# Performance work log

Measured on AMD Instinct MI355X. Metric: run time of the kernel, lower is better.

Reference implementation:

```python
import jax, jax.numpy as jnp
import numpy as np

N_NODES = 50000
N_EDGES = 800000
T_SEQ = 2048
H = 128  # LSTM hidden size


def _lstm_dir(x, w_ih, w_hh, b, reverse):
    # x: [T, Din]; torch gate order: i, f, g, o
    xg = x @ w_ih.T + b  # [T, 4H] precomputed input contribution
    h0 = jnp.zeros((H,), x.dtype)

    def step(carry, g_t):
        h, c = carry
        g = g_t + h @ w_hh.T
        i, f, gg, o = jnp.split(g, 4)
        i = jax.nn.sigmoid(i); f = jax.nn.sigmoid(f)
        gg = jnp.tanh(gg); o = jax.nn.sigmoid(o)
        c = f * c + i * gg
        h = o * jnp.tanh(c)
        return (h, c), h

    _, hs = jax.lax.scan(step, (h0, h0), xg, reverse=reverse)
    return hs  # [T, H], time-aligned with x


def _bilstm(x, layer_params):
    for (wif, whf, bf, wir, whr, br) in layer_params:
        hf = _lstm_dir(x, wif, whf, bf, reverse=False)
        hr = _lstm_dir(x, wir, whr, br, reverse=True)
        x = jnp.concatenate([hf, hr], axis=-1)
    return x  # [T, 2H]


def _forward(g_mol, feat_seq, edge_src, edge_dst, edge_weight, smiles_kmer,
             w_ih_l0, w_hh_l0, b_ih_l0, b_hh_l0,
             w_ih_l0_r, w_hh_l0_r, b_ih_l0_r, b_hh_l0_r,
             w_ih_l1, w_hh_l1, b_ih_l1, b_hh_l1,
             w_ih_l1_r, w_hh_l1_r, b_ih_l1_r, b_hh_l1_r,
             W1, b1, W2, b2,
             fc1_w, fc1_b, fc2_w, fc2_b, fc3_w, fc3_b, fc4_w, fc4_b):
    n = feat_seq.shape[0]
    # ---- BiLSTM encoder over the (unbatched) molecule sequence [T,17] ----
    layer_params = [
        (w_ih_l0, w_hh_l0, b_ih_l0 + b_hh_l0, w_ih_l0_r, w_hh_l0_r, b_ih_l0_r + b_hh_l0_r),
        (w_ih_l1, w_hh_l1, b_ih_l1 + b_hh_l1, w_ih_l1_r, w_hh_l1_r, b_ih_l1_r + b_hh_l1_r),
    ]
    lstm_out = _bilstm(g_mol, layer_params)              # [T, 256]
    g_mol_vec = lstm_out.mean(axis=0, keepdims=True)     # [1, 256] (mean over dim 0, keepdim)

    # ---- GraphConv 1 (norm='none'): weighted sum-aggregate src->dst, then linear ----
    msg = edge_weight[:, None] * feat_seq[edge_src]                # [E, 128]
    agg = jax.ops.segment_sum(msg, edge_dst, num_segments=n)      # [N, 128]
    h = jax.nn.relu(agg @ W1 + b1)
    # ---- GraphConv 2 ----
    msg2 = edge_weight[:, None] * h[edge_src]                      # [E, 128]
    agg2 = jax.ops.segment_sum(msg2, edge_dst, num_segments=n)    # [N, 128]
    h2 = agg2 @ W2 + b2                                            # [N, 256]
    hg_seq = h2.mean(axis=0, keepdims=True)                        # [1, 256] single-graph mean_nodes

    # ---- concat + MLP head ----
    features = jnp.concatenate([hg_seq, g_mol_vec, smiles_kmer], axis=1)  # [1, 1150]
    out = jax.nn.relu(features @ fc1_w.T + fc1_b)
    out = jax.nn.relu(out @ fc2_w.T + fc2_b)
    out = jax.nn.relu(out @ fc3_w.T + fc3_b)
    out = out @ fc4_w.T + fc4_b
    return out  # [1, 1]


def setup_inputs():
    key = jax.random.key(0)
    ks = iter(jax.random.split(key, 48))

    def rn(shape, s=0.05):
        return jax.random.normal(next(ks), shape, dtype=jnp.float32) * s

    inp = {}
    inp["g_mol"] = jax.random.normal(next(ks), (T_SEQ, 17), dtype=jnp.float32)
    inp["feat_seq"] = jax.random.normal(next(ks), (N_NODES, 128), dtype=jnp.float32)
    inp["edge_src"] = jax.random.randint(next(ks), (N_EDGES,), 0, N_NODES)
    inp["edge_dst"] = jax.random.randint(next(ks), (N_EDGES,), 0, N_NODES)
    inp["edge_weight"] = jax.random.uniform(next(ks), (N_EDGES,), dtype=jnp.float32)
    inp["smiles_kmer"] = jax.random.normal(next(ks), (1, 638), dtype=jnp.float32)
    for l, din in ((0, 17), (1, 2 * H)):
        for suf in ("", "_r"):
            inp[f"w_ih_l{l}{suf}"] = rn((4 * H, din))
            inp[f"w_hh_l{l}{suf}"] = rn((4 * H, H))
            inp[f"b_ih_l{l}{suf}"] = rn((4 * H,))
            inp[f"b_hh_l{l}{suf}"] = rn((4 * H,))
    inp["W1"] = rn((128, 128)); inp["b1"] = jnp.zeros((128,), jnp.float32)
    inp["W2"] = rn((128, 256)); inp["b2"] = jnp.zeros((256,), jnp.float32)
    inp["fc1_w"] = rn((575, 1150)); inp["fc1_b"] = jnp.zeros((575,), jnp.float32)
    inp["fc2_w"] = rn((256, 575)); inp["fc2_b"] = jnp.zeros((256,), jnp.float32)
    inp["fc3_w"] = rn((64, 256)); inp["fc3_b"] = jnp.zeros((64,), jnp.float32)
    inp["fc4_w"] = rn((1, 64)); inp["fc4_b"] = jnp.zeros((1,), jnp.float32)
    return inp


def reference(g_mol, feat_seq, edge_src, edge_dst, edge_weight, smiles_kmer,
              w_ih_l0, w_hh_l0, b_ih_l0, b_hh_l0,
              w_ih_l0_r, w_hh_l0_r, b_ih_l0_r, b_hh_l0_r,
              w_ih_l1, w_hh_l1, b_ih_l1, b_hh_l1,
              w_ih_l1_r, w_hh_l1_r, b_ih_l1_r, b_hh_l1_r,
              W1, b1, W2, b2,
              fc1_w, fc1_b, fc2_w, fc2_b, fc3_w, fc3_b, fc4_w, fc4_b):
    return _forward(g_mol, feat_seq, edge_src, edge_dst, edge_weight, smiles_kmer,
                    w_ih_l0, w_hh_l0, b_ih_l0, b_hh_l0,
                    w_ih_l0_r, w_hh_l0_r, b_ih_l0_r, b_hh_l0_r,
                    w_ih_l1, w_hh_l1, b_ih_l1, b_hh_l1,
                    w_ih_l1_r, w_hh_l1_r, b_ih_l1_r, b_hh_l1_r,
                    W1, b1, W2, b2,
                    fc1_w, fc1_b, fc2_w, fc2_b, fc3_w, fc3_b, fc4_w, fc4_b)
```

## Files before the change

kernel.cpp:

```cpp
#include <hip/hip_runtime.h>
#include <hip/hip_bf16.h>

#define T_SEQ 2048
#define HID 128
#define G4 512
#define N_NODES 50000
#define N_EDGES 800000

typedef float f32x4 __attribute__((ext_vector_type(4)));
typedef _Float16 f16x2 __attribute__((ext_vector_type(2)));
typedef _Float16 f16x8 __attribute__((ext_vector_type(8)));

__device__ __forceinline__ float fast_sigmoid(float x) {
    return 1.0f / (1.0f + __expf(-x));
}
__device__ __forceinline__ float fast_tanh(float x) {
    return 1.0f - 2.0f / (__expf(2.0f * x) + 1.0f);
}

__device__ __forceinline__ float dot2_f16(float bits_w, f16x2 h2, float acc) {
    f16x2 w2 = __builtin_bit_cast(f16x2, bits_w);
#if __has_builtin(__builtin_amdgcn_fdot2)
    return __builtin_amdgcn_fdot2(w2, h2, acc, false);
#else
    asm("v_dot2_f32_f16 %0, %1, %2, %0" : "+v"(acc) : "v"(w2), "v"(h2));
    return acc;
#endif
}

__global__ void xg0_kernel(const float* __restrict__ g_mol,
                           const float* __restrict__ wf, const float* __restrict__ bfi, const float* __restrict__ bfh,
                           const float* __restrict__ wr, const float* __restrict__ bri, const float* __restrict__ brh,
                           float* __restrict__ xg_f, float* __restrict__ xg_r)
{
    int gid = blockIdx.x * blockDim.x + threadIdx.x;
    int j = gid & (G4 - 1);
    int rest = gid >> 9;
    int t = rest & (T_SEQ - 1);
    int dir = rest >> 11;
    const float* w  = dir ? wr  : wf;
    const float* bi = dir ? bri : bfi;
    const float* bh = dir ? brh : bfh;
    float* xg = dir ? xg_r : xg_f;
    const float* x  = g_mol + t * 17;
    const float* wj = w + j * 17;
    float acc = bi[j] + bh[j];
    #pragma unroll
    for (int k = 0; k < 17; ++k) acc += x[k] * wj[k];
    xg[t * G4 + j] = acc;
}

struct ScanSmem {
    _Float16 h16[2][HID] __attribute__((aligned(16)));
    float g[G4];
    float part[G4];
};

#define B8(M) M(0,0,1,2,3) M(1,4,5,6,7) M(2,8,9,10,11) M(3,12,13,14,15) \
              M(4,16,17,18,19) M(5,20,21,22,23) M(6,24,25,26,27) M(7,28,29,30,31)
#define P32(M) M(0) M(1) M(2) M(3) M(4) M(5) M(6) M(7) M(8) M(9) M(10) M(11) \
               M(12) M(13) M(14) M(15) M(16) M(17) M(18) M(19) M(20) M(21) M(22) \
               M(23) M(24) M(25) M(26) M(27) M(28) M(29) M(30) M(31)

__device__ __forceinline__ void lstm_scan_dev(ScanSmem* sm, int dir,
                                              const float* __restrict__ xg,
                                              const float* __restrict__ whh,
                                              float* __restrict__ out,
                                              float* __restrict__ gvec, int write_out)
{
    const int tid = threadIdx.x;
    const int j = tid & (G4 - 1);
    const int half = tid >> 9;

    const float* wptr = whh + j * HID + half * 64;

#define DECL_PK(p) float apk##p; { \
    f16x2 pk_ = { (_Float16)wptr[2*(p)], (_Float16)wptr[2*(p)+1] }; \
    float bits_ = __builtin_bit_cast(float, pk_); \
    asm volatile("v_accvgpr_write_b32 %0, %1" : "=a"(apk##p) : "v"(bits_)); }
    P32(DECL_PK)
#undef DECL_PK

    if (tid < HID) sm->h16[0][tid] = (_Float16)0.0f;
    float c = 0.0f;
    float msum = 0.0f;
    __syncthreads();

    int t0 = dir ? (T_SEQ - 1) : 0;
    float xv = (half == 0) ? xg[t0 * G4 + j] : 0.0f;

    int pp = 0;
    for (int s = 0; s < T_SEQ; ++s) {
        int s2 = (s + 1 < T_SEQ) ? (s + 1) : s;
        int t      = dir ? (T_SEQ - 1 - s)  : s;
        int t_next = dir ? (T_SEQ - 1 - s2) : s2;
        float xv_n = (half == 0) ? xg[t_next * G4 + j] : 0.0f;

        const f16x8* h16v = reinterpret_cast<const f16x8*>(&sm->h16[pp][half * 64]);
        float acc0 = 0.f, acc1 = 0.f, acc2 = 0.f, acc3 = 0.f;
#define DOT_BLK(i, q0, q1, q2, q3) { f16x8 hv = h16v[i]; float b0_, b1_, b2_, b3_; \
        asm volatile("v_accvgpr_read_b32 %0, %1" : "=v"(b0_) : "a"(apk##q0)); \
        asm volatile("v_accvgpr_read_b32 %0, %1" : "=v"(b1_) : "a"(apk##q1)); \
        asm volatile("v_accvgpr_read_b32 %0, %1" : "=v"(b2_) : "a"(apk##q2)); \
        asm volatile("v_accvgpr_read_b32 %0, %1" : "=v"(b3_) : "a"(apk##q3)); \
        f16x2 h0_ = { hv[0], hv[1] }, h1_ = { hv[2], hv[3] }; \
        f16x2 h2_ = { hv[4], hv[5] }, h3_ = { hv[6], hv[7] }; \
        acc0 = dot2_f16(b0_, h0_, acc0); acc1 = dot2_f16(b1_, h1_, acc1); \
        acc2 = dot2_f16(b2_, h2_, acc2); acc3 = dot2_f16(b3_, h3_, acc3); }
        B8(DOT_BLK)
#undef DOT_BLK
        float p = (acc0 + acc1) + (acc2 + acc3);
        if (half) sm->part[j] = p;
        else      sm->g[j] = p + xv;
        __syncthreads();
        if (tid < HID) {
            float ig = fast_sigmoid(sm->g[tid]           + sm->part[tid]);
            float fg = fast_sigmoid(sm->g[HID + tid]     + sm->part[HID + tid]);
            float gg = fast_tanh(   sm->g[2 * HID + tid] + sm->part[2 * HID + tid]);
            float og = fast_sigmoid(sm->g[3 * HID + tid] + sm->part[3 * HID + tid]);
            c = fg * c + ig * gg;
            float hh = og * fast_tanh(c);
            sm->h16[pp ^ 1][tid] = (_Float16)hh;
            if (write_out) out[t * HID + tid] = hh;
            msum += hh;
        }
        __syncthreads();
        pp ^= 1;
        xv = xv_n;
    }
    if (gvec != nullptr && tid < HID) gvec[dir * HID + tid] = msum * (1.0f / (float)T_SEQ);
}

#define SCAT_BLOCKS ((N_EDGES * 32) / 1024)
__global__ __launch_bounds__(1024, 1)
void combined1(const float* __restrict__ xg_f, const float* __restrict__ xg_r,
               const float* __restrict__ whh_f, const float* __restrict__ whh_r,
               float* __restrict__ out_f, float* __restrict__ out_r,
               const int* __restrict__ esrc, const int* __restrict__ edst,
               const float* __restrict__ ew, const float* __restrict__ feat,
               float* __restrict__ agg)
{
    __shared__ ScanSmem ssm;
    __shared__ float pad_iso[19456];
    volatile float* vpad = pad_iso;
    vpad[threadIdx.x] = 0.0f;
    int bid = blockIdx.x;
    if (bid < 2) {
        lstm_scan_dev(&ssm, bid, bid ? xg_r : xg_f, bid ? whh_r : whh_f,
                      bid ? out_r : out_f, nullptr, 1);
        return;
    }
    int gid = (bid - 2) * 1024 + threadIdx.x;
    int e = gid >> 5;
    int c = gid & 31;
    int s = esrc[e], d = edst[e];
    float w = ew[e];
    float4 v = reinterpret_cast<const float4*>(feat)[(long)s * 32 + c];
    float* ap = agg + (long)d * HID + (c << 2);
    atomicAdd(ap + 0, w * v.x);
    atomicAdd(ap + 1, w * v.y);
    atomicAdd(ap + 2, w * v.z);
    atomicAdd(ap + 3, w * v.w);
}

#define XG1_BLOCKS 512
#define NPB2 96
#define G1_BLOCKS ((N_NODES + NPB2 - 1) / NPB2)
__global__ __launch_bounds__(1024, 1)
void combined2(const float* __restrict__ hf0, const float* __restrict__ hr0,
               const float* __restrict__ wf, const float* __restrict__ bfi, const float* __restrict__ bfh,
               const float* __restrict__ wr, const float* __restrict__ bri, const float* __restrict__ brh,
               float* __restrict__ xg_f, float* __restrict__ xg_r,
               const float* __restrict__ W1, const float* __restrict__ b1,
               float* __restrict__ agg)
{
    __shared__ float w_s[128 * 128];
    __shared__ float row_s[8][HID];
    int bid = blockIdx.x;
    int tid = threadIdx.x;
    if (bid < XG1_BLOCKS) {
        int gid = bid * 1024 + tid;
        int j = gid & (G4 - 1);
        int rest = gid >> 9;
        int tb = rest & 511;
        int dir = rest >> 9;
        const float* w  = dir ? wr  : wf;
        const float* bi = dir ? bri : bfi;
        const float* bh = dir ? brh : bfh;
        float* xg = dir ? xg_r : xg_f;
        int t0 = tb * 4;

        float b = bi[j] + bh[j];
        float a0 = b, a1 = b, a2 = b, a3 = b;
        const float4* wrow = reinterpret_cast<const float4*>(w + j * 256);
        const float4* hf = reinterpret_cast<const float4*>(hf0 + t0 * HID);
        const float4* hr = reinterpret_cast<const float4*>(hr0 + t0 * HID);
        #pragma unroll 8
        for (int k = 0; k < 32; ++k) {
            float4 wv = wrow[k];
            float4 v0 = hf[k], v1 = hf[32 + k], v2 = hf[64 + k], v3 = hf[96 + k];
            a0 += wv.x*v0.x + wv.y*v0.y + wv.z*v0.z + wv.w*v0.w;
            a1 += wv.x*v1.x + wv.y*v1.y + wv.z*v1.z + wv.w*v1.w;
            a2 += wv.x*v2.x + wv.y*v2.y + wv.z*v2.z + wv.w*v2.w;
            a3 += wv.x*v3.x + wv.y*v3.y + wv.z*v3.z + wv.w*v3.w;
        }
        #pragma unroll 8
        for (int k = 0; k < 32; ++k) {
            float4 wv = wrow[32 + k];
            float4 v0 = hr[k], v1 = hr[32 + k], v2 = hr[64 + k], v3 = hr[96 + k];
            a0 += wv.x*v0.x + wv.y*v0.y + wv.z*v0.z + wv.w*v0.w;
            a1 += wv.x*v1.x + wv.y*v1.y + wv.z*v1.z + wv.w*v1.w;
            a2 += wv.x*v2.x + wv.y*v2.y + wv.z*v2.z + wv.w*v2.w;
            a3 += wv.x*v3.x + wv.y*v3.y + wv.z*v3.z + wv.w*v3.w;
        }
        xg[(t0 + 0) * G4 + j] = a0;
        xg[(t0 + 1) * G4 + j] = a1;
        xg[(t0 + 2) * G4 + j] = a2;
        xg[(t0 + 3) * G4 + j] = a3;
        return;
    }
    int gb = bid - XG1_BLOCKS;
    int j = tid & 127;
    int sub = tid >> 7;
    for (int i = tid; i < 128 * 128; i += 1024) w_s[i] = W1[i];
    float bj = b1[j];
    __syncthreads();
    int base = gb * NPB2;
    for (int n0 = base; n0 < base + NPB2; n0 += 8) {
        int row = n0 + sub;
        bool valid = row < N_NODES;
        if (valid) row_s[sub][j] = agg[(long)row * HID + j];
        __syncthreads();
        float a = bj;
        #pragma unroll 8
        for (int k = 0; k < 128; ++k) a += row_s[sub][k] * w_s[k * 128 + j];
        __syncthreads();
        if (valid) agg[(long)row * HID + j] = fmaxf(a, 0.0f);
    }
}

#define HOP2_BLOCKS 1024
__global__ __launch_bounds__(1024, 4)
void combined3(const float* __restrict__ xg_f, const float* __restrict__ xg_r,
               const float* __restrict__ whh_f, const float* __restrict__ whh_r,
               float* __restrict__ gvec,
               const int* __restrict__ esrc, const float* __restrict__ ew,
               const float* __restrict__ h, float* __restrict__ s_out)
{
    __shared__ ScanSmem ssm;
    __shared__ float red[1024 * 4];
    int bid = blockIdx.x;
    int tid = threadIdx.x;
    if (bid < 2) {
        lstm_scan_dev(&ssm, bid, bid ? xg_r : xg_f, bid ? whh_r : whh_f,
                      nullptr, gvec, 0);
        return;
    }
    int hb = bid - 2;
    int c = tid & 31;
    int g = tid >> 5;
    float ax = 0.f, ay = 0.f, az = 0.f, aw = 0.f;
    const float4* h4 = reinterpret_cast<const float4*>(h);
    for (long e = (long)hb * 32 + g; e < N_EDGES; e += (long)HOP2_BLOCKS * 32) {
        float wgt = ew[e];
        int sidx = esrc[e];
        float4 v = h4[(long)sidx * 32 + c];
        ax += wgt * v.x; ay += wgt * v.y; az += wgt * v.z; aw += wgt * v.w;
    }
    red[tid * 4 + 0] = ax; red[tid * 4 + 1] = ay;
    red[tid * 4 + 2] = az; red[tid * 4 + 3] = aw;
    __syncthreads();
    if (tid < 32) {
        float r0 = 0.f, r1 = 0.f, r2 = 0.f, r3 = 0.f;
        for (int gg = 0; gg < 32; ++gg) {
            int b = (gg * 32 + tid) * 4;
            r0 += red[b + 0]; r1 += red[b + 1]; r2 += red[b + 2]; r3 += red[b + 3];
        }
        atomicAdd(&s_out[tid * 4 + 0], r0);
        atomicAdd(&s_out[tid * 4 + 1], r1);
        atomicAdd(&s_out[tid * 4 + 2], r2);
        atomicAdd(&s_out[tid * 4 + 3], r3);
    }
}

__global__ __launch_bounds__(640)
void head_kernel(const float* __restrict__ s_in, const float* __restrict__ W2, const float* __restrict__ b2,
                 const float* __restrict__ gvec, const float* __restrict__ kmer,
                 const float* __restrict__ fc1w, const float* __restrict__ fc1b,
                 const float* __restrict__ fc2w, const float* __restrict__ fc2b,
                 const float* __restrict__ fc3w, const float* __restrict__ fc3b,
                 const float* __restrict__ fc4w, const float* __restrict__ fc4b,
                 float* __restrict__ out)
{
    __shared__ float feat[1152];
    __shared__ float a1[576];
    __shared__ float a2[256];
    __shared__ float a3[64];
    int tid = threadIdx.x;
    if (tid < 256) {
        float acc = b2[tid];
        const float inv_n = 1.0f / (float)N_NODES;
        for (int k = 0; k < HID; ++k)
            acc += (s_in[k] * inv_n) * W2[k * 256 + tid];
        feat[tid] = acc;
    } else if (tid < 512) {
        feat[tid] = gvec[tid - 256];
    }
    if (tid < 638) feat[512 + tid] = kmer[tid];
    __syncthreads();

    if (tid < 575) {
        const float2* wr = reinterpret_cast<const float2*>(fc1w + (long)tid * 1150);
        const float2* f2 = reinterpret_cast<const float2*>(feat);
        float acc = fc1b[tid];
        for (int k = 0; k < 575; ++k) {
            float2 wv = wr[k]; float2 fv = f2[k];
            acc += wv.x * fv.x + wv.y * fv.y;
        }
        a1[tid] = fmaxf(acc, 0.0f);
    }
    __syncthreads();
    if (tid < 256) {
        const float* wr = fc2w + (long)tid * 575;
        float acc = fc2b[tid];
        for (int k = 0; k < 575; ++k) acc += a1[k] * wr[k];
        a2[tid] = fmaxf(acc, 0.0f);
    }
    __syncthreads();
    if (tid < 64) {
        const float4* wr = reinterpret_cast<const float4*>(fc3w + (long)tid * 256);
        const float4* av4 = reinterpret_cast<const float4*>(a2);
        float acc = fc3b[tid];
        for (int k = 0; k < 64; ++k) {
            float4 wv = wr[k]; float4 av = av4[k];
            acc += wv.x*av.x + wv.y*av.y + wv.z*av.z + wv.w*av.w;
        }
        a3[tid] = fmaxf(acc, 0.0f);
    }
    __syncthreads();
    if (tid == 0) {
        float acc = fc4b[0];
        for (int k = 0; k < 64; ++k) acc += a3[k] * fc4w[k];
        out[0] = acc;
    }
}

extern "C" void kernel_launch(void* const* d_in, const int* in_sizes, int n_in,
                              void* d_out, int out_size, void* d_ws, size_t ws_size,
                              hipStream_t stream)
{
    const float* g_mol = (const float*)d_in[0];
    const float* feat  = (const float*)d_in[1];
    const int*   esrc  = (const int*)d_in[2];
    const int*   edst  = (const int*)d_in[3];
    const float* ew    = (const float*)d_in[4];
    const float* kmer  = (const float*)d_in[5];
    const float* w_ih_l0  = (const float*)d_in[6];
    const float* w_hh_l0  = (const float*)d_in[7];
    const float* b_ih_l0  = (const float*)d_in[8];
    const float* b_hh_l0  = (const float*)d_in[9];
    const float* w_ih_l0r = (const float*)d_in[10];
    const float* w_hh_l0r = (const float*)d_in[11];
    const float* b_ih_l0r = (const float*)d_in[12];
    const float* b_hh_l0r = (const float*)d_in[13];
    const float* w_ih_l1  = (const float*)d_in[14];
    const float* w_hh_l1  = (const float*)d_in[15];
    const float* b_ih_l1  = (const float*)d_in[16];
    const float* b_hh_l1  = (const float*)d_in[17];
    const float* w_ih_l1r = (const float*)d_in[18];
    const float* w_hh_l1r = (const float*)d_in[19];
    const float* b_ih_l1r = (const float*)d_in[20];
    const float* b_hh_l1r = (const float*)d_in[21];
    const float* W1 = (const float*)d_in[22];
    const float* b1 = (const float*)d_in[23];
    const float* W2 = (const float*)d_in[24];
    const float* b2 = (const float*)d_in[25];
    const float* fc1w = (const float*)d_in[26];
    const float* fc1b = (const float*)d_in[27];
    const float* fc2w = (const float*)d_in[28];
    const float* fc2b = (const float*)d_in[29];
    const float* fc3w = (const float*)d_in[30];
    const float* fc3b = (const float*)d_in[31];
    const float* fc4w = (const float*)d_in[32];
    const float* fc4b = (const float*)d_in[33];

    float* ws  = (float*)d_ws;
    float* XGF  = ws;
    float* XGR  = XGF + T_SEQ * G4;
    float* HF0  = XGR + T_SEQ * G4;
    float* HR0  = HF0 + T_SEQ * HID;
    float* GVEC = HR0 + T_SEQ * HID;
    float* SUM  = GVEC + 256;
    float* AGG  = SUM + 128;

    hipMemsetAsync(AGG, 0, (size_t)N_NODES * HID * sizeof(float), stream);
    hipMemsetAsync(SUM, 0, 128 * sizeof(float), stream);

    xg0_kernel<<<(2 * T_SEQ * G4) / 256, 256, 0, stream>>>(
        g_mol, w_ih_l0, b_ih_l0, b_hh_l0, w_ih_l0r, b_ih_l0r, b_hh_l0r, XGF, XGR);

    combined1<<<2 + SCAT_BLOCKS, 1024, 0, stream>>>(
        XGF, XGR, w_hh_l0, w_hh_l0r, HF0, HR0, esrc, edst, ew, feat, AGG);

    combined2<<<XG1_BLOCKS + G1_BLOCKS, 1024, 0, stream>>>(
        HF0, HR0, w_ih_l1, b_ih_l1, b_hh_l1, w_ih_l1r, b_ih_l1r, b_hh_l1r,
        XGF, XGR, W1, b1, AGG);

    combined3<<<2 + HOP2_BLOCKS, 1024, 0, stream>>>(
        XGF, XGR, w_hh_l1, w_hh_l1r, GVEC, esrc, ew, AGG, SUM);

    head_kernel<<<1, 640, 0, stream>>>(SUM, W2, b2, GVEC, kmer,
                                       fc1w, fc1b, fc2w, fc2b, fc3w, fc3b, fc4w, fc4b,
                                       (float*)d_out);
}
```

Baseline: 5.097 ms.

## Build CSR by destination for gather aggregation and collapse hop-2 via out-weights

Adds histogram, prefix-scan and reorder kernels that build a destination-sorted CSR, along with per-source out-weight sums. The first GraphConv becomes an atomic-free gather per node, which also removes the large AGG memset. The second hop's edge gather is replaced by an algebraically equivalent node-level weighted reduction with outw[n]. The cost is three extra serial kernels before the LSTM/graph overlap kernels start, and the graph work was already overlapped with the sequential LSTM scans.

```diff
diff --git a/kernel.cpp b/kernel.cpp
--- a/kernel.cpp
+++ b/kernel.cpp
@@ -48,6 +48,55 @@
     #pragma unroll
     for (int k = 0; k < 17; ++k) acc += x[k] * wj[k];
     xg[t * G4 + j] = acc;
+}
+
+#define EDGE_BLOCKS ((N_EDGES + 1023) / 1024)
+__global__ void hist_kernel(const int* __restrict__ esrc, const int* __restrict__ edst,
+                            const float* __restrict__ ew,
+                            int* __restrict__ cnt, float* __restrict__ outw)
+{
+    int e = blockIdx.x * 1024 + threadIdx.x;
+    if (e < N_EDGES) {
+        atomicAdd(&cnt[edst[e]], 1);
+        atomicAdd(&outw[esrc[e]], ew[e]);
+    }
+}
+
+__global__ __launch_bounds__(1024)
+void prefix_kernel(const int* __restrict__ cnt, int* __restrict__ offs, int* __restrict__ cursor)
+{
+    __shared__ int part[1024];
+    const int tid = threadIdx.x;
+    const int CH = (N_NODES + 1023) / 1024;
+    int base = tid * CH;
+    int sum = 0;
+    for (int i = 0; i < CH; ++i) { int idx = base + i; if (idx < N_NODES) sum += cnt[idx]; }
+    part[tid] = sum;
+    __syncthreads();
+    for (int d = 1; d < 1024; d <<= 1) {
+        int v = (tid >= d) ? part[tid - d] : 0;
+        __syncthreads();
+        part[tid] += v;
+        __syncthreads();
+    }
+    int run = (tid == 0) ? 0 : part[tid - 1];
+    for (int i = 0; i < CH; ++i) {
+        int idx = base + i;
+        if (idx < N_NODES) { offs[idx] = run; cursor[idx] = run; run += cnt[idx]; }
+    }
+    if (tid == 1023) offs[N_NODES] = run;
+}
+
+__global__ void reorder_kernel(const int* __restrict__ esrc, const int* __restrict__ edst,
+                               const float* __restrict__ ew, int* __restrict__ cursor,
+                               int* __restrict__ csr_src, float* __restrict__ csr_w)
+{
+    int e = blockIdx.x * 1024 + threadIdx.x;
+    if (e < N_EDGES) {
+        int pos = atomicAdd(&cursor[edst[e]], 1);
+        csr_src[pos] = esrc[e];
+        csr_w[pos]   = ew[e];
+    }
 }
 
 struct ScanSmem {
@@ -131,13 +180,13 @@
     if (gvec != nullptr && tid < HID) gvec[dir * HID + tid] = msum * (1.0f / (float)T_SEQ);
 }
 
-#define SCAT_BLOCKS ((N_EDGES * 32) / 1024)
+#define GATHER_BLOCKS (N_NODES / 16)
 __global__ __launch_bounds__(1024, 1)
 void combined1(const float* __restrict__ xg_f, const float* __restrict__ xg_r,
                const float* __restrict__ whh_f, const float* __restrict__ whh_r,
                float* __restrict__ out_f, float* __restrict__ out_r,
-               const int* __restrict__ esrc, const int* __restrict__ edst,
-               const float* __restrict__ ew, const float* __restrict__ feat,
+               const int* __restrict__ offs, const int* __restrict__ csr_src,
+               const float* __restrict__ csr_w, const float* __restrict__ feat,
                float* __restrict__ agg)
 {
     __shared__ ScanSmem ssm;
@@ -145,22 +194,25 @@
     volatile float* vpad = pad_iso;
     vpad[threadIdx.x] = 0.0f;
     int bid = blockIdx.x;
+    int tid = threadIdx.x;
     if (bid < 2) {
         lstm_scan_dev(&ssm, bid, bid ? xg_r : xg_f, bid ? whh_r : whh_f,
                       bid ? out_r : out_f, nullptr, 1);
         return;
     }
-    int gid = (bid - 2) * 1024 + threadIdx.x;
-    int e = gid >> 5;
-    int c = gid & 31;
-    int s = esrc[e], d = edst[e];
-    float w = ew[e];
-    float4 v = reinterpret_cast<const float4*>(feat)[(long)s * 32 + c];
-    float* ap = agg + (long)d * HID + (c << 2);
-    atomicAdd(ap + 0, w * v.x);
-    atomicAdd(ap + 1, w * v.y);
-    atomicAdd(ap + 2, w * v.z);
-    atomicAdd(ap + 3, w * v.w);
+    int n = (bid - 2) * 16 + (tid >> 6);
+    int lane = tid & 63;
+    int start = offs[n], end = offs[n + 1];
+    float ax = 0.0f, ay = 0.0f;
+    const float2* f2 = reinterpret_cast<const float2*>(feat);
+    for (int e = start; e < end; ++e) {
+        int src = csr_src[e];
+        float wgt = csr_w[e];
+        float2 v = f2[(long)src * 64 + lane];
+        ax += wgt * v.x; ay += wgt * v.y;
+    }
+    float2 o; o.x = ax; o.y = ay;
+    reinterpret_cast<float2*>(agg)[(long)n * 64 + lane] = o;
 }
 
 #define XG1_BLOCKS 512
@@ -239,16 +291,16 @@
     }
 }
 
-#define HOP2_BLOCKS 1024
+#define RED_BLOCKS 512
 __global__ __launch_bounds__(1024, 4)
 void combined3(const float* __restrict__ xg_f, const float* __restrict__ xg_r,
                const float* __restrict__ whh_f, const float* __restrict__ whh_r,
                float* __restrict__ gvec,
-               const int* __restrict__ esrc, const float* __restrict__ ew,
-               const float* __restrict__ h, float* __restrict__ s_out)
+               const float* __restrict__ outw, const float* __restrict__ h,
+               float* __restrict__ s_out)
 {
     __shared__ ScanSmem ssm;
-    __shared__ float red[1024 * 4];
+    __shared__ float red[8 * 128];
     int bid = blockIdx.x;
     int tid = threadIdx.x;
     if (bid < 2) {
@@ -257,29 +309,18 @@
         return;
     }
     int hb = bid - 2;
-    int c = tid & 31;
-    int g = tid >> 5;
-    float ax = 0.f, ay = 0.f, az = 0.f, aw = 0.f;
-    const float4* h4 = reinterpret_cast<const float4*>(h);
-    for (long e = (long)hb * 32 + g; e < N_EDGES; e += (long)HOP2_BLOCKS * 32) {
-        float wgt = ew[e];
-        int sidx = esrc[e];
-        float4 v = h4[(long)sidx * 32 + c];
-        ax += wgt * v.x; ay += wgt * v.y; az += wgt * v.z; aw += wgt * v.w;
-    }
-    red[tid * 4 + 0] = ax; red[tid * 4 + 1] = ay;
-    red[tid * 4 + 2] = az; red[tid * 4 + 3] = aw;
-    __syncthreads();
-    if (tid < 32) {
-        float r0 = 0.f, r1 = 0.f, r2 = 0.f, r3 = 0.f;
-        for (int gg = 0; gg < 32; ++gg) {
-            int b = (gg * 32 + tid) * 4;
-            r0 += red[b + 0]; r1 += red[b + 1]; r2 += red[b + 2]; r3 += red[b + 3];
-        }
-        atomicAdd(&s_out[tid * 4 + 0], r0);
-        atomicAdd(&s_out[tid * 4 + 1], r1);
-        atomicAdd(&s_out[tid * 4 + 2], r2);
-        atomicAdd(&s_out[tid * 4 + 3], r3);
+    int f = tid & 127;
+    int r = tid >> 7;
+    float acc = 0.0f;
+    for (int n = hb * 8 + r; n < N_NODES; n += RED_BLOCKS * 8)
+        acc += outw[n] * h[(long)n * HID + f];
+    red[r * 128 + f] = acc;
+    __syncthreads();
+    if (tid < 128) {
+        float s = 0.0f;
+        #pragma unroll
+        for (int rr = 0; rr < 8; ++rr) s += red[rr * 128 + tid];
+        atomicAdd(&s_out[tid], s);
     }
 }
 
@@ -392,22 +433,33 @@
     float* GVEC = HR0 + T_SEQ * HID;
     float* SUM  = GVEC + 256;
     float* AGG  = SUM + 128;
-
-    hipMemsetAsync(AGG, 0, (size_t)N_NODES * HID * sizeof(float), stream);
+    float* OUTW = AGG + (size_t)N_NODES * HID;
+    float* CSRW = OUTW + N_NODES;
+    int*   CNT  = (int*)(CSRW + N_EDGES);
+    int*   OFFS = CNT + (N_NODES + 4);
+    int*   CURS = OFFS + (N_NODES + 4);
+    int*   CSRS = CURS + (N_NODES + 4);
+
     hipMemsetAsync(SUM, 0, 128 * sizeof(float), stream);
+    hipMemsetAsync(OUTW, 0, N_NODES * sizeof(float), stream);
+    hipMemsetAsync(CNT, 0, (N_NODES + 4) * sizeof(int), stream);
+
+    hist_kernel<<<EDGE_BLOCKS, 1024, 0, stream>>>(esrc, edst, ew, CNT, OUTW);
+    prefix_kernel<<<1, 1024, 0, stream>>>(CNT, OFFS, CURS);
+    reorder_kernel<<<EDGE_BLOCKS, 1024, 0, stream>>>(esrc, edst, ew, CURS, CSRS, CSRW);
 
     xg0_kernel<<<(2 * T_SEQ * G4) / 256, 256, 0, stream>>>(
         g_mol, w_ih_l0, b_ih_l0, b_hh_l0, w_ih_l0r, b_ih_l0r, b_hh_l0r, XGF, XGR);
 
-    combined1<<<2 + SCAT_BLOCKS, 1024, 0, stream>>>(
-        XGF, XGR, w_hh_l0, w_hh_l0r, HF0, HR0, esrc, edst, ew, feat, AGG);
+    combined1<<<2 + GATHER_BLOCKS, 1024, 0, stream>>>(
+        XGF, XGR, w_hh_l0, w_hh_l0r, HF0, HR0, OFFS, CSRS, CSRW, feat, AGG);
 
     combined2<<<XG1_BLOCKS + G1_BLOCKS, 1024, 0, stream>>>(
         HF0, HR0, w_ih_l1, b_ih_l1, b_hh_l1, w_ih_l1r, b_ih_l1r, b_hh_l1r,
         XGF, XGR, W1, b1, AGG);
 
-    combined3<<<2 + HOP2_BLOCKS, 1024, 0, stream>>>(
-        XGF, XGR, w_hh_l1, w_hh_l1r, GVEC, esrc, ew, AGG, SUM);
+    combined3<<<2 + RED_BLOCKS, 1024, 0, stream>>>(
+        XGF, XGR, w_hh_l1, w_hh_l1r, GVEC, OUTW, AGG, SUM);
 
     head_kernel<<<1, 640, 0, stream>>>(SUM, W2, b2, GVEC, kmer,
                                        fc1w, fc1b, fc2w, fc2b, fc3w, fc3b, fc4w, fc4b,
```

After: 4.589 ms. 1.11x faster.
